# Optimization experiments

Measured on AMD Instinct MI355X. Metric: run time of the kernel, lower is better.

The kernel has to match this reference:

```python
import jax, jax.numpy as jnp
import numpy as np

C = 256
HEADS = 8
HD = C // HEADS
EPS = 1e-5


def _layernorm(x, g, b):
    mu = jnp.mean(x, axis=-1, keepdims=True)
    var = jnp.var(x, axis=-1, keepdims=True)
    return (x - mu) * jax.lax.rsqrt(var + EPS) * g + b


def setup_inputs() -> dict:
    key = jax.random.key(0)
    ks = jax.random.split(key, 16)
    s = 0.02
    return {
        "x": jax.random.normal(ks[0], (1, C, 64, 64), jnp.float32),
        "bn_gamma": 1.0 + s * jax.random.normal(ks[1], (C,), jnp.float32),
        "bn_beta": s * jax.random.normal(ks[2], (C,), jnp.float32),
        "bn_mean": s * jax.random.normal(ks[3], (C,), jnp.float32),
        "bn_var": jnp.ones((C,), jnp.float32),
        "w_in": s * jax.random.normal(ks[4], (C, C), jnp.float32),
        "b_in": jnp.zeros((C,), jnp.float32),
        "ln1_g": jnp.ones((C,), jnp.float32),
        "ln1_b": jnp.zeros((C,), jnp.float32),
        "w_qkv": s * jax.random.normal(ks[5], (3 * C, C), jnp.float32),
        "b_qkv": jnp.zeros((3 * C,), jnp.float32),
        "w_ap": s * jax.random.normal(ks[6], (C, C), jnp.float32),
        "b_ap": jnp.zeros((C,), jnp.float32),
        "ln2_g": jnp.ones((C,), jnp.float32),
        "ln2_b": jnp.zeros((C,), jnp.float32),
        "w_ff1": s * jax.random.normal(ks[7], (4 * C, C), jnp.float32),
        "b_ff1": jnp.zeros((4 * C,), jnp.float32),
        "w_ff2": s * jax.random.normal(ks[8], (C, 4 * C), jnp.float32),
        "b_ff2": jnp.zeros((C,), jnp.float32),
        "w_out": s * jax.random.normal(ks[9], (C, C), jnp.float32),
        "b_out": jnp.zeros((C,), jnp.float32),
    }


def reference(x, bn_gamma, bn_beta, bn_mean, bn_var, w_in, b_in,
              ln1_g, ln1_b, w_qkv, b_qkv, w_ap, b_ap,
              ln2_g, ln2_b, w_ff1, b_ff1, w_ff2, b_ff2, w_out, b_out):
    b, c, h, w = x.shape
    t = h * w
    x_in = x
    # BatchNorm2d (eval mode: running stats)
    xn = (x - bn_mean[None, :, None, None]) * jax.lax.rsqrt(bn_var + EPS)[None, :, None, None]
    xn = xn * bn_gamma[None, :, None, None] + bn_beta[None, :, None, None]
    # proj_in 1x1 conv -> tokens [b, t, c]
    tok = xn.reshape(b, c, t).transpose(0, 2, 1)
    tok = tok @ w_in.T + b_in
    # transformer block (depth=1)
    y = _layernorm(tok, ln1_g, ln1_b)  # norm1
    qkv = y @ w_qkv.T + b_qkv  # [b, t, 3c], channel split (3, H, hd)
    qkv = qkv.reshape(b, t, 3, HEADS, HD)
    q = qkv[:, :, 0].transpose(0, 2, 1, 3)  # [b, H, t, hd]
    k = qkv[:, :, 1].transpose(0, 2, 1, 3)
    v = qkv[:, :, 2].transpose(0, 2, 1, 3)
    scale = HD ** (-0.5)
    attn = jax.nn.softmax(jnp.einsum('bhqd,bhkd->bhqk', q, k) * scale, axis=-1)
    o = jnp.einsum('bhqk,bhkd->bhqd', attn, v)  # [b, H, t, hd]
    o = o.transpose(0, 2, 1, 3).reshape(b, t, c)  # channels ordered (H, hd)
    o = o @ w_ap.T + b_ap  # attn proj 1x1
    attn_out = o + y  # VanillaAttention residual adds its (normed) input
    tok = tok + attn_out
    # FFN
    z = _layernorm(tok, ln2_g, ln2_b)
    z = jax.nn.gelu(z @ w_ff1.T + b_ff1, approximate=False)
    tok = tok + (z @ w_ff2.T + b_ff2)
    # back to image, proj_out 1x1, outer residual
    x4 = tok.transpose(0, 2, 1).reshape(b, c, h, w)
    out = jnp.einsum('oc,bchw->bohw', w_out, x4) + b_out[None, :, None, None]
    return out + x_in
```

## Files before the change

kernel.cpp:

```cpp
#include <hip/hip_runtime.h>
#include <math.h>

#define T_TOK 4096
#define C_DIM 256
#define EPSF  1e-5f
#define SC_QL (0.17677669529663687f * 1.4426950408889634f)

typedef short  bf16x8  __attribute__((ext_vector_type(8)));
typedef float  f32x4   __attribute__((ext_vector_type(4)));
typedef ushort ushort8 __attribute__((ext_vector_type(8)));

__device__ __forceinline__ short f2bf(float f) {
    unsigned u = __builtin_bit_cast(unsigned, f);
    unsigned r = (u + 0x7FFFu + ((u >> 16) & 1u)) >> 16;
    return (short)r;
}
__device__ __forceinline__ unsigned pk_bf16(float a, float b) {
    const unsigned ua = __builtin_bit_cast(unsigned, a) + 0x8000u;
    const unsigned ub = __builtin_bit_cast(unsigned, b) + 0x8000u;
    return __builtin_amdgcn_perm(ub, ua, 0x07060302u);
}

__global__ __launch_bounds__(256) void prep_kernel(
    const float* __restrict__ w_in, const float* __restrict__ w_qkv,
    const float* __restrict__ w_ap, const float* __restrict__ w_ff1,
    const float* __restrict__ w_ff2, const float* __restrict__ w_out,
    const float* __restrict__ b_qkv, ushort* __restrict__ wbuf,
    float* __restrict__ bqs,
    const float* __restrict__ x, const float* __restrict__ gamma,
    const float* __restrict__ beta, const float* __restrict__ mean,
    const float* __restrict__ var, ushort* __restrict__ tin)
{
    __shared__ float tile[32][33];
    if (blockIdx.x < 896) {
        const int gid = blockIdx.x * 256 + threadIdx.x;
        const int e0 = gid * 4;
        const float* src; int off; float sc = 1.f;
        if (e0 < 65536)       { src = w_in;  off = e0; }
        else if (e0 < 262144) { src = w_qkv; off = e0 - 65536; if (off < 65536) sc = SC_QL; }
        else if (e0 < 327680) { src = w_ap;  off = e0 - 262144; }
        else if (e0 < 589824) { src = w_ff1; off = e0 - 327680; }
        else if (e0 < 851968) { src = w_ff2; off = e0 - 589824; }
        else                  { src = w_out; off = e0 - 851968; }
        const float4 v = *(const float4*)(src + off);
        ushort4 o;
        o.x = (ushort)f2bf(v.x * sc); o.y = (ushort)f2bf(v.y * sc);
        o.z = (ushort)f2bf(v.z * sc); o.w = (ushort)f2bf(v.w * sc);
        *(ushort4*)(wbuf + e0) = o;
        if (gid < 192) {
            const float s2 = (gid < 64) ? SC_QL : 1.f;
            float4 b = ((const float4*)b_qkv)[gid];
            b.x *= s2; b.y *= s2; b.z *= s2; b.w *= s2;
            ((float4*)bqs)[gid] = b;
        }
    } else {
        const int bidx = blockIdx.x - 896;
        const int t0 = (bidx & 127) * 32, c0 = (bidx >> 7) * 32;
        const int tx = threadIdx.x & 31, ty = threadIdx.x >> 5;
#pragma unroll
        for (int i = 0; i < 32; i += 8) {
            const int c = c0 + ty + i;
            const float a = rsqrtf(var[c] + EPSF) * gamma[c];
            const float d = beta[c] - mean[c] * a;
            tile[ty + i][tx] = x[c * T_TOK + t0 + tx] * a + d;
        }
        __syncthreads();
#pragma unroll
        for (int i = 0; i < 32; i += 8) {
            const int t = t0 + ty + i;
            tin[t * C_DIM + c0 + tx] = (ushort)f2bf(tile[tx][ty + i]);
        }
    }
}

template <bool WRITE_F32>
__global__ __launch_bounds__(256) void ln_kernel(
    const float* __restrict__ in, const float* __restrict__ g,
    const float* __restrict__ b, float* __restrict__ outF,
    ushort* __restrict__ outB)
{
    const int wave = threadIdx.x >> 6, lane = threadIdx.x & 63;
    const int row = (blockIdx.x << 2) + wave;
    const float4 v = *(const float4*)(in + row * C_DIM + lane * 4);
    float s  = v.x + v.y + v.z + v.w;
    float s2 = v.x * v.x + v.y * v.y + v.z * v.z + v.w * v.w;
#pragma unroll
    for (int off = 32; off > 0; off >>= 1) {
        s  += __shfl_xor(s, off);
        s2 += __shfl_xor(s2, off);
    }
    const float mu  = s * (1.0f / C_DIM);
    const float varr = s2 * (1.0f / C_DIM) - mu * mu;
    const float rs  = rsqrtf(varr + EPSF);
    const float4 gv = *(const float4*)(g + lane * 4);
    const float4 bv = *(const float4*)(b + lane * 4);
    float4 o;
    o.x = (v.x - mu) * rs * gv.x + bv.x;
    o.y = (v.y - mu) * rs * gv.y + bv.y;
    o.z = (v.z - mu) * rs * gv.z + bv.z;
    o.w = (v.w - mu) * rs * gv.w + bv.w;
    if (WRITE_F32) *(float4*)(outF + row * C_DIM + lane * 4) = o;
    ushort4 ob;
    ob.x = (ushort)f2bf(o.x); ob.y = (ushort)f2bf(o.y);
    ob.z = (ushort)f2bf(o.z); ob.w = (ushort)f2bf(o.w);
    *(ushort4*)(outB + row * C_DIM + lane * 4) = ob;
}

template <int MODE>
__global__ __launch_bounds__(512) void gemm_bf(
    const ushort* __restrict__ A, const ushort* __restrict__ W,
    const float* __restrict__ bias, const float* __restrict__ add1,
    const float* __restrict__ add2, const float* __restrict__ xin,
    float* __restrict__ outF, ushort* __restrict__ outB,
    int M, int N, int K)
{
    __shared__ ushort As[2][2][64 * 40];
    __shared__ ushort Ws[2][2][64 * 40];
    __shared__ f32x4  Cred[4][64][4];
    const int m0 = blockIdx.x * 64, n0 = blockIdx.y * 64;
    const int tid = threadIdx.x;
    const int wv = tid >> 6, lane = tid & 63;
    const int half = wv >> 2, wl = wv & 3;
    const int c16 = lane & 15, g = lane >> 4;
    const int ht = tid & 255;
    const int r = ht >> 2, cc8 = (ht & 3) * 8;
    const int Kh = K >> 1;

    const ushort* Ap = A + (size_t)(m0 + r) * K + half * Kh + cc8;
    const ushort* Wp = W + (size_t)(n0 + r) * K + half * Kh + cc8;
    ushort8 apre = *(const ushort8*)Ap;
    ushort8 wpre = *(const ushort8*)Wp;

    f32x4 acc[4] = {};
    int p = 0;
    for (int k0 = 0; k0 < Kh; k0 += 32) {
        *(ushort8*)&As[half][p][r * 40 + cc8] = apre;
        *(ushort8*)&Ws[half][p][r * 40 + cc8] = wpre;
        __syncthreads();
        if (k0 + 32 < Kh) {
            apre = *(const ushort8*)(Ap + k0 + 32);
            wpre = *(const ushort8*)(Wp + k0 + 32);
        }
        const bf16x8 af = *(const bf16x8*)&As[half][p][(wl * 16 + c16) * 40 + g * 8];
#pragma unroll
        for (int nf = 0; nf < 4; ++nf) {
            const bf16x8 bfv = *(const bf16x8*)&Ws[half][p][(nf * 16 + c16) * 40 + g * 8];
            acc[nf] = __builtin_amdgcn_mfma_f32_16x16x32_bf16(af, bfv, acc[nf], 0, 0, 0);
        }
        p ^= 1;
    }

    __syncthreads();
    if (half == 1) {
#pragma unroll
        for (int nf = 0; nf < 4; ++nf) Cred[wl][lane][nf] = acc[nf];
    }
    __syncthreads();
    if (half == 0) {
#pragma unroll
        for (int nf = 0; nf < 4; ++nf) {
            const f32x4 t = Cred[wl][lane][nf];
#pragma unroll
            for (int rr = 0; rr < 4; ++rr) acc[nf][rr] += t[rr];
        }
        const int row0 = m0 + wl * 16 + g * 4;
#pragma unroll
        for (int nf = 0; nf < 4; ++nf) {
            const int col = n0 + nf * 16 + c16;
            const float bc = (MODE == 5) ? 0.f : bias[col];
#pragma unroll
            for (int rr = 0; rr < 4; ++rr) {
                const int row = row0 + rr;
                const size_t idx = (size_t)row * N + col;
                float v = acc[nf][rr] + bc;
                if (MODE == 5) v += bias[row] + xin[idx];
                if (MODE == 2) v += add1[idx] + add2[idx];
                if (MODE == 4) v += add1[idx];
                if (MODE == 3) v = 0.5f * v * (1.0f + erff(v * 0.70710678118654752f));
                if (MODE == 0 || MODE == 2 || MODE == 5) outF[idx] = v;
                else outB[idx] = (ushort)f2bf(v);
            }
        }
    }
}

#define KS   40
#define VTS  72
#define PS_W 36

__global__ __launch_bounds__(256) void attn_mfma(
    const ushort* __restrict__ qkv, ushort* __restrict__ o)
{
    const int h   = blockIdx.y;
    const int q0  = blockIdx.x << 6;
    const int tid = threadIdx.x;
    const int wv  = tid >> 6, lane = tid & 63;
    const int c   = lane & 15, g = lane >> 4;

    __shared__ ushort Ks[2][64 * KS];
    __shared__ ushort Vt[2][32 * VTS];
    __shared__ float  Ps[4][16 * PS_W];

    const bf16x8 qf = *(const bf16x8*)(qkv + (size_t)(q0 + wv * 16 + c) * 768 + h * 32 + g * 8);

    bf16x8 ones;
#pragma unroll
    for (int i = 0; i < 8; ++i) ones[i] = (short)0x3F80;

    f32x4 oacc0 = {0.f, 0.f, 0.f, 0.f};
    f32x4 oacc1 = {0.f, 0.f, 0.f, 0.f};
    f32x4 oaccl = {0.f, 0.f, 0.f, 0.f};

    const int kr = tid >> 2, kc = (tid & 3) * 8;
    const int vp = tid & 31, vd = (tid >> 5) * 4;
    const ushort* kbase = qkv + 256 + h * 32;
    const ushort* vbase = qkv + 512 + h * 32;

    ushort8 kpre  = *(const ushort8*)(kbase + (size_t)kr * 768 + kc);
    ushort4 vpre0 = *(const ushort4*)(vbase + (size_t)(2 * vp) * 768 + vd);
    ushort4 vpre1 = *(const ushort4*)(vbase + (size_t)(2 * vp + 1) * 768 + vd);

    int p = 0;
    for (int kt = 0; kt < 64; ++kt) {
        *(ushort8*)&Ks[p][kr * KS + kc] = kpre;
        {
            unsigned* vtp = (unsigned*)&Vt[p][0];
            vtp[(vd + 0) * (VTS / 2) + vp] = (unsigned)vpre0.x | ((unsigned)vpre1.x << 16);
            vtp[(vd + 1) * (VTS / 2) + vp] = (unsigned)vpre0.y | ((unsigned)vpre1.y << 16);
            vtp[(vd + 2) * (VTS / 2) + vp] = (unsigned)vpre0.z | ((unsigned)vpre1.z << 16);
            vtp[(vd + 3) * (VTS / 2) + vp] = (unsigned)vpre0.w | ((unsigned)vpre1.w << 16);
        }
        __syncthreads();
        if (kt < 63) {
            const size_t t0 = (size_t)(kt + 1) * 64;
            kpre  = *(const ushort8*)(kbase + (t0 + kr) * 768 + kc);
            vpre0 = *(const ushort4*)(vbase + (t0 + 2 * vp) * 768 + vd);
            vpre1 = *(const ushort4*)(vbase + (t0 + 2 * vp + 1) * 768 + vd);
        }

        const ushort* ks = &Ks[p][0];
        const ushort* vt = &Vt[p][0];
        const f32x4 zz = {0.f, 0.f, 0.f, 0.f};
        const bf16x8 k0 = *(const bf16x8*)&ks[(0 * 16 + c) * KS + g * 8];
        const bf16x8 k1 = *(const bf16x8*)&ks[(1 * 16 + c) * KS + g * 8];
        const bf16x8 k2 = *(const bf16x8*)&ks[(2 * 16 + c) * KS + g * 8];
        const bf16x8 k3 = *(const bf16x8*)&ks[(3 * 16 + c) * KS + g * 8];
        const f32x4 s0 = __builtin_amdgcn_mfma_f32_16x16x32_bf16(k0, qf, zz, 0, 0, 0);
        const f32x4 s1 = __builtin_amdgcn_mfma_f32_16x16x32_bf16(k1, qf, zz, 0, 0, 0);
        const f32x4 s2 = __builtin_amdgcn_mfma_f32_16x16x32_bf16(k2, qf, zz, 0, 0, 0);
        const f32x4 s3 = __builtin_amdgcn_mfma_f32_16x16x32_bf16(k3, qf, zz, 0, 0, 0);

        float* prow = &Ps[wv][c * PS_W];
        {
            const float e00 = __builtin_amdgcn_exp2f(s0[0]), e01 = __builtin_amdgcn_exp2f(s0[1]);
            const float e02 = __builtin_amdgcn_exp2f(s0[2]), e03 = __builtin_amdgcn_exp2f(s0[3]);
            const float e10 = __builtin_amdgcn_exp2f(s1[0]), e11 = __builtin_amdgcn_exp2f(s1[1]);
            const float e12 = __builtin_amdgcn_exp2f(s1[2]), e13 = __builtin_amdgcn_exp2f(s1[3]);
            const float e20 = __builtin_amdgcn_exp2f(s2[0]), e21 = __builtin_amdgcn_exp2f(s2[1]);
            const float e22 = __builtin_amdgcn_exp2f(s2[2]), e23 = __builtin_amdgcn_exp2f(s2[3]);
            const float e30 = __builtin_amdgcn_exp2f(s3[0]), e31 = __builtin_amdgcn_exp2f(s3[1]);
            const float e32 = __builtin_amdgcn_exp2f(s3[2]), e33 = __builtin_amdgcn_exp2f(s3[3]);
            prow[0 * 8 + 2 * g + 0] = __builtin_bit_cast(float, pk_bf16(e00, e01));
            prow[0 * 8 + 2 * g + 1] = __builtin_bit_cast(float, pk_bf16(e02, e03));
            prow[1 * 8 + 2 * g + 0] = __builtin_bit_cast(float, pk_bf16(e10, e11));
            prow[1 * 8 + 2 * g + 1] = __builtin_bit_cast(float, pk_bf16(e12, e13));
            prow[2 * 8 + 2 * g + 0] = __builtin_bit_cast(float, pk_bf16(e20, e21));
            prow[2 * 8 + 2 * g + 1] = __builtin_bit_cast(float, pk_bf16(e22, e23));
            prow[3 * 8 + 2 * g + 0] = __builtin_bit_cast(float, pk_bf16(e30, e31));
            prow[3 * 8 + 2 * g + 1] = __builtin_bit_cast(float, pk_bf16(e32, e33));
        }

#pragma unroll
        for (int ch = 0; ch < 2; ++ch) {
            const bf16x8 pf = *(const bf16x8*)&prow[ch * 16 + 4 * g];
            const bf16x8 v0 = *(const bf16x8*)&vt[(c)      * VTS + ch * 32 + g * 8];
            const bf16x8 v1 = *(const bf16x8*)&vt[(16 + c) * VTS + ch * 32 + g * 8];
            oacc0 = __builtin_amdgcn_mfma_f32_16x16x32_bf16(pf, v0, oacc0, 0, 0, 0);
            oacc1 = __builtin_amdgcn_mfma_f32_16x16x32_bf16(pf, v1, oacc1, 0, 0, 0);
            oaccl = __builtin_amdgcn_mfma_f32_16x16x32_bf16(pf, ones, oaccl, 0, 0, 0);
        }
        p ^= 1;
        __syncthreads();
    }

    {
        ushort* op = o + (size_t)(q0 + wv * 16) * 256 + h * 32;
#pragma unroll
        for (int rr = 0; rr < 4; ++rr) {
            const float inv = 1.f / oaccl[rr];
            op[(4 * g + rr) * 256 + c]      = (ushort)f2bf(oacc0[rr] * inv);
            op[(4 * g + rr) * 256 + 16 + c] = (ushort)f2bf(oacc1[rr] * inv);
        }
    }
}

extern "C" void kernel_launch(void* const* d_in, const int* in_sizes, int n_in,
                              void* d_out, int out_size, void* d_ws, size_t ws_size,
                              hipStream_t stream)
{
    const float* x     = (const float*)d_in[0];
    const float* bn_g  = (const float*)d_in[1];
    const float* bn_b  = (const float*)d_in[2];
    const float* bn_m  = (const float*)d_in[3];
    const float* bn_v  = (const float*)d_in[4];
    const float* w_in  = (const float*)d_in[5];
    const float* b_in  = (const float*)d_in[6];
    const float* ln1_g = (const float*)d_in[7];
    const float* ln1_b = (const float*)d_in[8];
    const float* w_qkv = (const float*)d_in[9];
    const float* b_qkv = (const float*)d_in[10];
    const float* w_ap  = (const float*)d_in[11];
    const float* b_ap  = (const float*)d_in[12];
    const float* ln2_g = (const float*)d_in[13];
    const float* ln2_b = (const float*)d_in[14];
    const float* w_ff1 = (const float*)d_in[15];
    const float* b_ff1 = (const float*)d_in[16];
    const float* w_ff2 = (const float*)d_in[17];
    const float* b_ff2 = (const float*)d_in[18];
    const float* w_out = (const float*)d_in[19];
    const float* b_out = (const float*)d_in[20];
    float* out = (float*)d_out;
    float* ws  = (float*)d_ws;

    const size_t MF = 1u << 20;
    float*  tok0    = ws;
    float*  y       = ws + MF;
    float*  tok1    = ws + 2 * MF;
    ushort* qkv_bf  = (ushort*)(ws + 3 * MF);
    ushort* zbuf_bf = (ushort*)(ws + 3 * MF);
    ushort* tin_bf  = (ushort*)(ws + 4 * MF + MF / 2);
    ushort* obuf_bf = tin_bf;
    ushort* y_bf    = (ushort*)(ws + 5 * MF);
    ushort* zin_bf  = y_bf;
    ushort* tok2_bf = (ushort*)(ws + MF);
    ushort* wbuf    = (ushort*)(ws + 5 * MF + MF / 2);
    const ushort* wb_in  = wbuf;
    const ushort* wb_qkv = wbuf + 65536;
    const ushort* wb_ap  = wbuf + 262144;
    const ushort* wb_ff1 = wbuf + 327680;
    const ushort* wb_ff2 = wbuf + 589824;
    const ushort* wb_out = wbuf + 851968;
    float* bqs = (float*)(wbuf + 917504);

    prep_kernel<<<1920, 256, 0, stream>>>(w_in, w_qkv, w_ap, w_ff1, w_ff2, w_out,
                                          b_qkv, wbuf, bqs,
                                          x, bn_g, bn_b, bn_m, bn_v, tin_bf);
    gemm_bf<0><<<dim3(64, 4), 512, 0, stream>>>(tin_bf, wb_in, b_in, nullptr, nullptr, nullptr,
                                                tok0, nullptr, 4096, 256, 256);
    ln_kernel<true><<<1024, 256, 0, stream>>>(tok0, ln1_g, ln1_b, y, y_bf);
    gemm_bf<1><<<dim3(64, 12), 512, 0, stream>>>(y_bf, wb_qkv, bqs, nullptr, nullptr, nullptr,
                                                 nullptr, qkv_bf, 4096, 768, 256);
    attn_mfma<<<dim3(64, 8), 256, 0, stream>>>(qkv_bf, obuf_bf);
    gemm_bf<2><<<dim3(64, 4), 512, 0, stream>>>(obuf_bf, wb_ap, b_ap, y, tok0, nullptr,
                                                tok1, nullptr, 4096, 256, 256);
    ln_kernel<false><<<1024, 256, 0, stream>>>(tok1, ln2_g, ln2_b, nullptr, zin_bf);
    gemm_bf<3><<<dim3(64, 16), 512, 0, stream>>>(zin_bf, wb_ff1, b_ff1, nullptr, nullptr, nullptr,
                                                 nullptr, zbuf_bf, 4096, 1024, 256);
    gemm_bf<4><<<dim3(64, 4), 512, 0, stream>>>(zbuf_bf, wb_ff2, b_ff2, tok1, nullptr, nullptr,
                                                nullptr, tok2_bf, 4096, 256, 1024);
    gemm_bf<5><<<dim3(4, 64), 512, 0, stream>>>(wb_out, tok2_bf, b_out, nullptr, nullptr, x,
                                                out, nullptr, 256, 4096, 256);
}
```

Baseline: 217.4 us.

## Fuse GEMM+LayerNorm chains into three row-tile kernels and split attention over keys

Replaces the separate GEMM and LayerNorm launches with three fused kernels that each process 16-token row tiles: proj_in+LN1+QKV, attn-proj+residual+LN2+FFN1+GELU, and FFN2+residual+proj_out. LayerNorm statistics are reduced in registers with DPP row sums and a small shared buffer. Attention is split across two key halves via a z grid dimension, writing unnormalized partial outputs and row sums that the next kernel combines. This cuts launch count and intermediate round trips and improves attention parallelism. In exchange, weights are read directly from global memory per block without LDS reuse, and only 256 blocks run the fused GEMMs.

Result: no change. 213.9 us (-1.6%).

```diff
diff --git a/kernel.cpp b/kernel.cpp
--- a/kernel.cpp
+++ b/kernel.cpp
@@ -15,11 +15,27 @@
     unsigned r = (u + 0x7FFFu + ((u >> 16) & 1u)) >> 16;
     return (short)r;
 }
+__device__ __forceinline__ float bf2f(ushort u) {
+    return __builtin_bit_cast(float, ((unsigned)u) << 16);
+}
 __device__ __forceinline__ unsigned pk_bf16(float a, float b) {
     const unsigned ua = __builtin_bit_cast(unsigned, a) + 0x8000u;
     const unsigned ub = __builtin_bit_cast(unsigned, b) + 0x8000u;
     return __builtin_amdgcn_perm(ub, ua, 0x07060302u);
 }
+template <int CTRL>
+__device__ __forceinline__ float dppf(float x) {
+    return __builtin_bit_cast(float,
+        __builtin_amdgcn_mov_dpp(__builtin_bit_cast(int, x), CTRL, 0xF, 0xF, true));
+}
+__device__ __forceinline__ float rowsum16(float x) {
+    x += dppf<0xB1>(x);
+    x += dppf<0x4E>(x);
+    x += dppf<0x141>(x);
+    x += dppf<0x140>(x);
+    return x;
+}
+#define MFMA16(a, b, c) __builtin_amdgcn_mfma_f32_16x16x32_bf16(a, b, c, 0, 0, 0)
 
 __global__ __launch_bounds__(256) void prep_kernel(
     const float* __restrict__ w_in, const float* __restrict__ w_qkv,
@@ -73,114 +89,106 @@
     }
 }
 
-template <bool WRITE_F32>
-__global__ __launch_bounds__(256) void ln_kernel(
-    const float* __restrict__ in, const float* __restrict__ g,
-    const float* __restrict__ b, float* __restrict__ outF,
-    ushort* __restrict__ outB)
+__global__ __launch_bounds__(256) void fused_pre(
+    const ushort* __restrict__ tin, const ushort* __restrict__ wb_in,
+    const float* __restrict__ b_in, const float* __restrict__ ln1_g,
+    const float* __restrict__ ln1_b, const ushort* __restrict__ wb_qkv,
+    const float* __restrict__ bqs, float* __restrict__ tok0,
+    float* __restrict__ yout, ushort* __restrict__ qkvb)
 {
-    const int wave = threadIdx.x >> 6, lane = threadIdx.x & 63;
-    const int row = (blockIdx.x << 2) + wave;
-    const float4 v = *(const float4*)(in + row * C_DIM + lane * 4);
-    float s  = v.x + v.y + v.z + v.w;
-    float s2 = v.x * v.x + v.y * v.y + v.z * v.z + v.w * v.w;
-#pragma unroll
-    for (int off = 32; off > 0; off >>= 1) {
-        s  += __shfl_xor(s, off);
-        s2 += __shfl_xor(s2, off);
-    }
-    const float mu  = s * (1.0f / C_DIM);
-    const float varr = s2 * (1.0f / C_DIM) - mu * mu;
-    const float rs  = rsqrtf(varr + EPSF);
-    const float4 gv = *(const float4*)(g + lane * 4);
-    const float4 bv = *(const float4*)(b + lane * 4);
-    float4 o;
-    o.x = (v.x - mu) * rs * gv.x + bv.x;
-    o.y = (v.y - mu) * rs * gv.y + bv.y;
-    o.z = (v.z - mu) * rs * gv.z + bv.z;
-    o.w = (v.w - mu) * rs * gv.w + bv.w;
-    if (WRITE_F32) *(float4*)(outF + row * C_DIM + lane * 4) = o;
-    ushort4 ob;
-    ob.x = (ushort)f2bf(o.x); ob.y = (ushort)f2bf(o.y);
-    ob.z = (ushort)f2bf(o.z); ob.w = (ushort)f2bf(o.w);
-    *(ushort4*)(outB + row * C_DIM + lane * 4) = ob;
-}
-
-template <int MODE>
-__global__ __launch_bounds__(512) void gemm_bf(
-    const ushort* __restrict__ A, const ushort* __restrict__ W,
-    const float* __restrict__ bias, const float* __restrict__ add1,
-    const float* __restrict__ add2, const float* __restrict__ xin,
-    float* __restrict__ outF, ushort* __restrict__ outB,
-    int M, int N, int K)
-{
-    __shared__ ushort As[2][2][64 * 40];
-    __shared__ ushort Ws[2][2][64 * 40];
-    __shared__ f32x4  Cred[4][64][4];
-    const int m0 = blockIdx.x * 64, n0 = blockIdx.y * 64;
-    const int tid = threadIdx.x;
-    const int wv = tid >> 6, lane = tid & 63;
-    const int half = wv >> 2, wl = wv & 3;
-    const int c16 = lane & 15, g = lane >> 4;
-    const int ht = tid & 255;
-    const int r = ht >> 2, cc8 = (ht & 3) * 8;
-    const int Kh = K >> 1;
-
-    const ushort* Ap = A + (size_t)(m0 + r) * K + half * Kh + cc8;
-    const ushort* Wp = W + (size_t)(n0 + r) * K + half * Kh + cc8;
-    ushort8 apre = *(const ushort8*)Ap;
-    ushort8 wpre = *(const ushort8*)Wp;
-
-    f32x4 acc[4] = {};
-    int p = 0;
-    for (int k0 = 0; k0 < Kh; k0 += 32) {
-        *(ushort8*)&As[half][p][r * 40 + cc8] = apre;
-        *(ushort8*)&Ws[half][p][r * 40 + cc8] = wpre;
-        __syncthreads();
-        if (k0 + 32 < Kh) {
-            apre = *(const ushort8*)(Ap + k0 + 32);
-            wpre = *(const ushort8*)(Wp + k0 + 32);
-        }
-        const bf16x8 af = *(const bf16x8*)&As[half][p][(wl * 16 + c16) * 40 + g * 8];
+    __shared__ ushort Atile[16 * 264];
+    __shared__ ushort Ytile[16 * 264];
+    __shared__ float  red[4][16][2];
+    const int t0 = blockIdx.x * 16;
+    const int tid = threadIdx.x, wv = tid >> 6, lane = tid & 63;
+    const int c = lane & 15, g = lane >> 4;
+
+    {
+        const int r = tid >> 4, c0 = (tid & 15) * 16;
+        const ushort8 a0 = *(const ushort8*)(tin + (size_t)(t0 + r) * 256 + c0);
+        const ushort8 a1 = *(const ushort8*)(tin + (size_t)(t0 + r) * 256 + c0 + 8);
+        *(ushort8*)&Atile[r * 264 + c0] = a0;
+        *(ushort8*)&Atile[r * 264 + c0 + 8] = a1;
+    }
+    __syncthreads();
+
+    f32x4 accp[4] = {};
+#pragma unroll 1
+    for (int kc = 0; kc < 8; ++kc) {
+        const bf16x8 af = *(const bf16x8*)&Atile[c * 264 + kc * 32 + g * 8];
 #pragma unroll
         for (int nf = 0; nf < 4; ++nf) {
-            const bf16x8 bfv = *(const bf16x8*)&Ws[half][p][(nf * 16 + c16) * 40 + g * 8];
-            acc[nf] = __builtin_amdgcn_mfma_f32_16x16x32_bf16(af, bfv, acc[nf], 0, 0, 0);
-        }
-        p ^= 1;
-    }
-
-    __syncthreads();
-    if (half == 1) {
-#pragma unroll
-        for (int nf = 0; nf < 4; ++nf) Cred[wl][lane][nf] = acc[nf];
-    }
-    __syncthreads();
-    if (half == 0) {
-#pragma unroll
-        for (int nf = 0; nf < 4; ++nf) {
-            const f32x4 t = Cred[wl][lane][nf];
-#pragma unroll
-            for (int rr = 0; rr < 4; ++rr) acc[nf][rr] += t[rr];
-        }
-        const int row0 = m0 + wl * 16 + g * 4;
-#pragma unroll
-        for (int nf = 0; nf < 4; ++nf) {
-            const int col = n0 + nf * 16 + c16;
-            const float bc = (MODE == 5) ? 0.f : bias[col];
-#pragma unroll
-            for (int rr = 0; rr < 4; ++rr) {
-                const int row = row0 + rr;
-                const size_t idx = (size_t)row * N + col;
-                float v = acc[nf][rr] + bc;
-                if (MODE == 5) v += bias[row] + xin[idx];
-                if (MODE == 2) v += add1[idx] + add2[idx];
-                if (MODE == 4) v += add1[idx];
-                if (MODE == 3) v = 0.5f * v * (1.0f + erff(v * 0.70710678118654752f));
-                if (MODE == 0 || MODE == 2 || MODE == 5) outF[idx] = v;
-                else outB[idx] = (ushort)f2bf(v);
-            }
-        }
+            const bf16x8 bfv = *(const bf16x8*)(wb_in +
+                (size_t)(wv * 64 + nf * 16 + c) * 256 + kc * 32 + g * 8);
+            accp[nf] = MFMA16(af, bfv, accp[nf]);
+        }
+    }
+    float vs[4][4];
+    float s1[4] = {}, s2[4] = {};
+#pragma unroll
+    for (int nf = 0; nf < 4; ++nf) {
+        const int col = wv * 64 + nf * 16 + c;
+        const float bb = b_in[col];
+#pragma unroll
+        for (int rr = 0; rr < 4; ++rr) {
+            const float v = accp[nf][rr] + bb;
+            vs[nf][rr] = v;
+            s1[rr] += v;
+            s2[rr] += v * v;
+            tok0[(size_t)(t0 + 4 * g + rr) * 256 + col] = v;
+        }
+    }
+#pragma unroll
+    for (int rr = 0; rr < 4; ++rr) { s1[rr] = rowsum16(s1[rr]); s2[rr] = rowsum16(s2[rr]); }
+    if (c == 0) {
+#pragma unroll
+        for (int rr = 0; rr < 4; ++rr) {
+            red[wv][4 * g + rr][0] = s1[rr];
+            red[wv][4 * g + rr][1] = s2[rr];
+        }
+    }
+    __syncthreads();
+    float mu[4], rs[4];
+#pragma unroll
+    for (int rr = 0; rr < 4; ++rr) {
+        const int row = 4 * g + rr;
+        const float S  = red[0][row][0] + red[1][row][0] + red[2][row][0] + red[3][row][0];
+        const float S2 = red[0][row][1] + red[1][row][1] + red[2][row][1] + red[3][row][1];
+        mu[rr] = S * (1.0f / 256.0f);
+        const float var = S2 * (1.0f / 256.0f) - mu[rr] * mu[rr];
+        rs[rr] = rsqrtf(var + EPSF);
+    }
+#pragma unroll
+    for (int nf = 0; nf < 4; ++nf) {
+        const int col = wv * 64 + nf * 16 + c;
+        const float gg = ln1_g[col], bb = ln1_b[col];
+#pragma unroll
+        for (int rr = 0; rr < 4; ++rr) {
+            const float yv = (vs[nf][rr] - mu[rr]) * rs[rr] * gg + bb;
+            yout[(size_t)(t0 + 4 * g + rr) * 256 + col] = yv;
+            Ytile[(4 * g + rr) * 264 + col] = (ushort)f2bf(yv);
+        }
+    }
+    __syncthreads();
+
+    f32x4 accq[12] = {};
+#pragma unroll 1
+    for (int kc = 0; kc < 8; ++kc) {
+        const bf16x8 af = *(const bf16x8*)&Ytile[c * 264 + kc * 32 + g * 8];
+#pragma unroll
+        for (int nf = 0; nf < 12; ++nf) {
+            const bf16x8 bfv = *(const bf16x8*)(wb_qkv +
+                (size_t)(wv * 192 + nf * 16 + c) * 256 + kc * 32 + g * 8);
+            accq[nf] = MFMA16(af, bfv, accq[nf]);
+        }
+    }
+#pragma unroll
+    for (int nf = 0; nf < 12; ++nf) {
+        const int col = wv * 192 + nf * 16 + c;
+        const float bb = bqs[col];
+#pragma unroll
+        for (int rr = 0; rr < 4; ++rr)
+            qkvb[(size_t)(t0 + 4 * g + rr) * 768 + col] = (ushort)f2bf(accq[nf][rr] + bb);
     }
 }
 
@@ -189,13 +197,15 @@
 #define PS_W 36
 
 __global__ __launch_bounds__(256) void attn_mfma(
-    const ushort* __restrict__ qkv, ushort* __restrict__ o)
+    const ushort* __restrict__ qkv, ushort* __restrict__ o1,
+    ushort* __restrict__ o2, float* __restrict__ lpart)
 {
-    const int h   = blockIdx.y;
-    const int q0  = blockIdx.x << 6;
-    const int tid = threadIdx.x;
-    const int wv  = tid >> 6, lane = tid & 63;
-    const int c   = lane & 15, g = lane >> 4;
+    const int h    = blockIdx.y;
+    const int q0   = blockIdx.x << 6;
+    const int half = blockIdx.z;
+    const int tid  = threadIdx.x;
+    const int wv   = tid >> 6, lane = tid & 63;
+    const int c    = lane & 15, g = lane >> 4;
 
     __shared__ ushort Ks[2][64 * KS];
     __shared__ ushort Vt[2][32 * VTS];
@@ -216,12 +226,13 @@
     const ushort* kbase = qkv + 256 + h * 32;
     const ushort* vbase = qkv + 512 + h * 32;
 
-    ushort8 kpre  = *(const ushort8*)(kbase + (size_t)kr * 768 + kc);
-    ushort4 vpre0 = *(const ushort4*)(vbase + (size_t)(2 * vp) * 768 + vd);
-    ushort4 vpre1 = *(const ushort4*)(vbase + (size_t)(2 * vp + 1) * 768 + vd);
+    const int kt0 = half * 32, kt1 = kt0 + 32;
+    ushort8 kpre  = *(const ushort8*)(kbase + ((size_t)kt0 * 64 + kr) * 768 + kc);
+    ushort4 vpre0 = *(const ushort4*)(vbase + ((size_t)kt0 * 64 + 2 * vp) * 768 + vd);
+    ushort4 vpre1 = *(const ushort4*)(vbase + ((size_t)kt0 * 64 + 2 * vp + 1) * 768 + vd);
 
     int p = 0;
-    for (int kt = 0; kt < 64; ++kt) {
+    for (int kt = kt0; kt < kt1; ++kt) {
         *(ushort8*)&Ks[p][kr * KS + kc] = kpre;
         {
             unsigned* vtp = (unsigned*)&Vt[p][0];
@@ -231,7 +242,7 @@
             vtp[(vd + 3) * (VTS / 2) + vp] = (unsigned)vpre0.w | ((unsigned)vpre1.w << 16);
         }
         __syncthreads();
-        if (kt < 63) {
+        if (kt + 1 < kt1) {
             const size_t t0 = (size_t)(kt + 1) * 64;
             kpre  = *(const ushort8*)(kbase + (t0 + kr) * 768 + kc);
             vpre0 = *(const ushort4*)(vbase + (t0 + 2 * vp) * 768 + vd);
@@ -245,10 +256,10 @@
         const bf16x8 k1 = *(const bf16x8*)&ks[(1 * 16 + c) * KS + g * 8];
         const bf16x8 k2 = *(const bf16x8*)&ks[(2 * 16 + c) * KS + g * 8];
         const bf16x8 k3 = *(const bf16x8*)&ks[(3 * 16 + c) * KS + g * 8];
-        const f32x4 s0 = __builtin_amdgcn_mfma_f32_16x16x32_bf16(k0, qf, zz, 0, 0, 0);
-        const f32x4 s1 = __builtin_amdgcn_mfma_f32_16x16x32_bf16(k1, qf, zz, 0, 0, 0);
-        const f32x4 s2 = __builtin_amdgcn_mfma_f32_16x16x32_bf16(k2, qf, zz, 0, 0, 0);
-        const f32x4 s3 = __builtin_amdgcn_mfma_f32_16x16x32_bf16(k3, qf, zz, 0, 0, 0);
+        const f32x4 s0 = MFMA16(k0, qf, zz);
+        const f32x4 s1 = MFMA16(k1, qf, zz);
+        const f32x4 s2 = MFMA16(k2, qf, zz);
+        const f32x4 s3 = MFMA16(k3, qf, zz);
 
         float* prow = &Ps[wv][c * PS_W];
         {
@@ -269,27 +280,224 @@
             prow[3 * 8 + 2 * g + 0] = __builtin_bit_cast(float, pk_bf16(e30, e31));
             prow[3 * 8 + 2 * g + 1] = __builtin_bit_cast(float, pk_bf16(e32, e33));
         }
-
 #pragma unroll
         for (int ch = 0; ch < 2; ++ch) {
             const bf16x8 pf = *(const bf16x8*)&prow[ch * 16 + 4 * g];
             const bf16x8 v0 = *(const bf16x8*)&vt[(c)      * VTS + ch * 32 + g * 8];
             const bf16x8 v1 = *(const bf16x8*)&vt[(16 + c) * VTS + ch * 32 + g * 8];
-            oacc0 = __builtin_amdgcn_mfma_f32_16x16x32_bf16(pf, v0, oacc0, 0, 0, 0);
-            oacc1 = __builtin_amdgcn_mfma_f32_16x16x32_bf16(pf, v1, oacc1, 0, 0, 0);
-            oaccl = __builtin_amdgcn_mfma_f32_16x16x32_bf16(pf, ones, oaccl, 0, 0, 0);
+            oacc0 = MFMA16(pf, v0, oacc0);
+            oacc1 = MFMA16(pf, v1, oacc1);
+            oaccl = MFMA16(pf, ones, oaccl);
         }
         p ^= 1;
         __syncthreads();
     }
 
     {
-        ushort* op = o + (size_t)(q0 + wv * 16) * 256 + h * 32;
-#pragma unroll
-        for (int rr = 0; rr < 4; ++rr) {
-            const float inv = 1.f / oaccl[rr];
-            op[(4 * g + rr) * 256 + c]      = (ushort)f2bf(oacc0[rr] * inv);
-            op[(4 * g + rr) * 256 + 16 + c] = (ushort)f2bf(oacc1[rr] * inv);
+        ushort* op = (half ? o2 : o1) + (size_t)(q0 + wv * 16) * 256 + h * 32;
+#pragma unroll
+        for (int rr = 0; rr < 4; ++rr) {
+            op[(4 * g + rr) * 256 + c]      = (ushort)f2bf(oacc0[rr]);
+            op[(4 * g + rr) * 256 + 16 + c] = (ushort)f2bf(oacc1[rr]);
+        }
+        if (c == 0) {
+#pragma unroll
+            for (int rr = 0; rr < 4; ++rr)
+                lpart[(size_t)(q0 + wv * 16 + 4 * g + rr) * 16 + half * 8 + h] = oaccl[rr];
+        }
+    }
+}
+
+__global__ __launch_bounds__(256) void fused_mid(
+    const ushort* __restrict__ o1, const ushort* __restrict__ o2,
+    const float* __restrict__ lpart, const ushort* __restrict__ wb_ap,
+    const float* __restrict__ b_ap, const float* __restrict__ yin,
+    const float* __restrict__ tok0, const float* __restrict__ ln2_g,
+    const float* __restrict__ ln2_b, const ushort* __restrict__ wb_ff1,
+    const float* __restrict__ b_ff1, float* __restrict__ tok1,
+    ushort* __restrict__ zbuf)
+{
+    __shared__ ushort Otile[16 * 264];
+    __shared__ ushort Ztile[16 * 264];
+    __shared__ float  red[4][16][2];
+    const int t0 = blockIdx.x * 16;
+    const int tid = threadIdx.x, wv = tid >> 6, lane = tid & 63;
+    const int c = lane & 15, g = lane >> 4;
+
+    {
+        const int r = tid >> 4, c0 = (tid & 15) * 16;
+        const int h = (tid & 15) >> 1;
+        const float inv = 1.0f / (lpart[(size_t)(t0 + r) * 16 + h] +
+                                  lpart[(size_t)(t0 + r) * 16 + 8 + h]);
+        const ushort8 a0 = *(const ushort8*)(o1 + (size_t)(t0 + r) * 256 + c0);
+        const ushort8 a1 = *(const ushort8*)(o1 + (size_t)(t0 + r) * 256 + c0 + 8);
+        const ushort8 b0 = *(const ushort8*)(o2 + (size_t)(t0 + r) * 256 + c0);
+        const ushort8 b1 = *(const ushort8*)(o2 + (size_t)(t0 + r) * 256 + c0 + 8);
+        unsigned w[4];
+#pragma unroll
+        for (int i = 0; i < 4; ++i) {
+            const float v0 = (bf2f(a0[2 * i]) + bf2f(b0[2 * i])) * inv;
+            const float v1 = (bf2f(a0[2 * i + 1]) + bf2f(b0[2 * i + 1])) * inv;
+            w[i] = pk_bf16(v0, v1);
+        }
+        *(ushort8*)&Otile[r * 264 + c0] = *(ushort8*)w;
+#pragma unroll
+        for (int i = 0; i < 4; ++i) {
+            const float v0 = (bf2f(a1[2 * i]) + bf2f(b1[2 * i])) * inv;
+            const float v1 = (bf2f(a1[2 * i + 1]) + bf2f(b1[2 * i + 1])) * inv;
+            w[i] = pk_bf16(v0, v1);
+        }
+        *(ushort8*)&Otile[r * 264 + c0 + 8] = *(ushort8*)w;
+    }
+    __syncthreads();
+
+    f32x4 accp[4] = {};
+#pragma unroll 1
+    for (int kc = 0; kc < 8; ++kc) {
+        const bf16x8 af = *(const bf16x8*)&Otile[c * 264 + kc * 32 + g * 8];
+#pragma unroll
+        for (int nf = 0; nf < 4; ++nf) {
+            const bf16x8 bfv = *(const bf16x8*)(wb_ap +
+                (size_t)(wv * 64 + nf * 16 + c) * 256 + kc * 32 + g * 8);
+            accp[nf] = MFMA16(af, bfv, accp[nf]);
+        }
+    }
+    float vs[4][4];
+    float s1[4] = {}, s2[4] = {};
+#pragma unroll
+    for (int nf = 0; nf < 4; ++nf) {
+        const int col = wv * 64 + nf * 16 + c;
+        const float bb = b_ap[col];
+#pragma unroll
+        for (int rr = 0; rr < 4; ++rr) {
+            const size_t idx = (size_t)(t0 + 4 * g + rr) * 256 + col;
+            const float v = accp[nf][rr] + bb + yin[idx] + tok0[idx];
+            vs[nf][rr] = v;
+            s1[rr] += v;
+            s2[rr] += v * v;
+            tok1[idx] = v;
+        }
+    }
+#pragma unroll
+    for (int rr = 0; rr < 4; ++rr) { s1[rr] = rowsum16(s1[rr]); s2[rr] = rowsum16(s2[rr]); }
+    if (c == 0) {
+#pragma unroll
+        for (int rr = 0; rr < 4; ++rr) {
+            red[wv][4 * g + rr][0] = s1[rr];
+            red[wv][4 * g + rr][1] = s2[rr];
+        }
+    }
+    __syncthreads();
+    float mu[4], rs[4];
+#pragma unroll
+    for (int rr = 0; rr < 4; ++rr) {
+        const int row = 4 * g + rr;
+        const float S  = red[0][row][0] + red[1][row][0] + red[2][row][0] + red[3][row][0];
+        const float S2 = red[0][row][1] + red[1][row][1] + red[2][row][1] + red[3][row][1];
+        mu[rr] = S * (1.0f / 256.0f);
+        const float var = S2 * (1.0f / 256.0f) - mu[rr] * mu[rr];
+        rs[rr] = rsqrtf(var + EPSF);
+    }
+#pragma unroll
+    for (int nf = 0; nf < 4; ++nf) {
+        const int col = wv * 64 + nf * 16 + c;
+        const float gg = ln2_g[col], bb = ln2_b[col];
+#pragma unroll
+        for (int rr = 0; rr < 4; ++rr) {
+            const float zv = (vs[nf][rr] - mu[rr]) * rs[rr] * gg + bb;
+            Ztile[(4 * g + rr) * 264 + col] = (ushort)f2bf(zv);
+        }
+    }
+    __syncthreads();
+
+    f32x4 accf[16] = {};
+#pragma unroll 1
+    for (int kc = 0; kc < 8; ++kc) {
+        const bf16x8 af = *(const bf16x8*)&Ztile[c * 264 + kc * 32 + g * 8];
+#pragma unroll
+        for (int nf = 0; nf < 16; ++nf) {
+            const bf16x8 bfv = *(const bf16x8*)(wb_ff1 +
+                (size_t)(wv * 256 + nf * 16 + c) * 256 + kc * 32 + g * 8);
+            accf[nf] = MFMA16(af, bfv, accf[nf]);
+        }
+    }
+#pragma unroll
+    for (int nf = 0; nf < 16; ++nf) {
+        const int col = wv * 256 + nf * 16 + c;
+        const float bb = b_ff1[col];
+#pragma unroll
+        for (int rr = 0; rr < 4; ++rr) {
+            float v = accf[nf][rr] + bb;
+            v = 0.5f * v * (1.0f + erff(v * 0.70710678118654752f));
+            zbuf[(size_t)(t0 + 4 * g + rr) * 1024 + col] = (ushort)f2bf(v);
+        }
+    }
+}
+
+__global__ __launch_bounds__(256) void fused_post(
+    const ushort* __restrict__ zbuf, const ushort* __restrict__ wb_ff2,
+    const float* __restrict__ b_ff2, const float* __restrict__ tok1,
+    const ushort* __restrict__ wb_out, const float* __restrict__ b_out,
+    const float* __restrict__ x, float* __restrict__ out)
+{
+    __shared__ ushort Ztile[16 * 1032];
+    __shared__ ushort T2tile[16 * 264];
+    const int t0 = blockIdx.x * 16;
+    const int tid = threadIdx.x, wv = tid >> 6, lane = tid & 63;
+    const int c = lane & 15, g = lane >> 4;
+
+    {
+        const int r = tid >> 4, c0 = (tid & 15) * 64;
+#pragma unroll
+        for (int i = 0; i < 8; ++i) {
+            const ushort8 zv = *(const ushort8*)(zbuf + (size_t)(t0 + r) * 1024 + c0 + i * 8);
+            *(ushort8*)&Ztile[r * 1032 + c0 + i * 8] = zv;
+        }
+    }
+    __syncthreads();
+
+    f32x4 accf[4] = {};
+#pragma unroll 1
+    for (int kc = 0; kc < 32; ++kc) {
+        const bf16x8 af = *(const bf16x8*)&Ztile[c * 1032 + kc * 32 + g * 8];
+#pragma unroll
+        for (int nf = 0; nf < 4; ++nf) {
+            const bf16x8 bfv = *(const bf16x8*)(wb_ff2 +
+                (size_t)(wv * 64 + nf * 16 + c) * 1024 + kc * 32 + g * 8);
+            accf[nf] = MFMA16(af, bfv, accf[nf]);
+        }
+    }
+#pragma unroll
+    for (int nf = 0; nf < 4; ++nf) {
+        const int col = wv * 64 + nf * 16 + c;
+        const float bb = b_ff2[col];
+#pragma unroll
+        for (int rr = 0; rr < 4; ++rr) {
+            const size_t idx = (size_t)(t0 + 4 * g + rr) * 256 + col;
+            const float v = accf[nf][rr] + bb + tok1[idx];
+            T2tile[(4 * g + rr) * 264 + col] = (ushort)f2bf(v);
+        }
+    }
+    __syncthreads();
+
+    f32x4 acco[4] = {};
+#pragma unroll 1
+    for (int kc = 0; kc < 8; ++kc) {
+        const bf16x8 bfr = *(const bf16x8*)&T2tile[c * 264 + kc * 32 + g * 8];
+#pragma unroll
+        for (int mf = 0; mf < 4; ++mf) {
+            const bf16x8 afr = *(const bf16x8*)(wb_out +
+                (size_t)(wv * 64 + mf * 16 + c) * 256 + kc * 32 + g * 8);
+            acco[mf] = MFMA16(afr, bfr, acco[mf]);
+        }
+    }
+#pragma unroll
+    for (int mf = 0; mf < 4; ++mf) {
+#pragma unroll
+        for (int rr = 0; rr < 4; ++rr) {
+            const int och = wv * 64 + mf * 16 + 4 * g + rr;
+            const size_t idx = (size_t)och * T_TOK + t0 + c;
+            out[idx] = acco[mf][rr] + b_out[och] + x[idx];
         }
     }
 }
@@ -323,17 +531,16 @@
     float* ws  = (float*)d_ws;
 
     const size_t MF = 1u << 20;
-    float*  tok0    = ws;
-    float*  y       = ws + MF;
-    float*  tok1    = ws + 2 * MF;
-    ushort* qkv_bf  = (ushort*)(ws + 3 * MF);
-    ushort* zbuf_bf = (ushort*)(ws + 3 * MF);
-    ushort* tin_bf  = (ushort*)(ws + 4 * MF + MF / 2);
-    ushort* obuf_bf = tin_bf;
-    ushort* y_bf    = (ushort*)(ws + 5 * MF);
-    ushort* zin_bf  = y_bf;
-    ushort* tok2_bf = (ushort*)(ws + MF);
-    ushort* wbuf    = (ushort*)(ws + 5 * MF + MF / 2);
+    float*  tok0   = ws;
+    float*  y      = ws + MF;
+    float*  tok1   = ws + 2 * MF;
+    ushort* qkv_bf = (ushort*)(ws + 3 * MF);
+    ushort* zbuf   = (ushort*)(ws + 4 * MF + MF / 2);
+    ushort* tin_bf = (ushort*)(ws + 6 * MF + MF / 2);
+    ushort* o1p    = tin_bf;
+    ushort* o2p    = (ushort*)(ws + 7 * MF);
+    float*  lpart  = ws + 7 * MF + MF / 2;
+    ushort* wbuf   = (ushort*)(ws + 7 * MF + MF / 2 + 65536);
     const ushort* wb_in  = wbuf;
     const ushort* wb_qkv = wbuf + 65536;
     const ushort* wb_ap  = wbuf + 262144;
@@ -345,19 +552,11 @@
     prep_kernel<<<1920, 256, 0, stream>>>(w_in, w_qkv, w_ap, w_ff1, w_ff2, w_out,
                                           b_qkv, wbuf, bqs,
                                           x, bn_g, bn_b, bn_m, bn_v, tin_bf);
-    gemm_bf<0><<<dim3(64, 4), 512, 0, stream>>>(tin_bf, wb_in, b_in, nullptr, nullptr, nullptr,
-                                                tok0, nullptr, 4096, 256, 256);
-    ln_kernel<true><<<1024, 256, 0, stream>>>(tok0, ln1_g, ln1_b, y, y_bf);
-    gemm_bf<1><<<dim3(64, 12), 512, 0, stream>>>(y_bf, wb_qkv, bqs, nullptr, nullptr, nullptr,
-                                                 nullptr, qkv_bf, 4096, 768, 256);
-    attn_mfma<<<dim3(64, 8), 256, 0, stream>>>(qkv_bf, obuf_bf);
-    gemm_bf<2><<<dim3(64, 4), 512, 0, stream>>>(obuf_bf, wb_ap, b_ap, y, tok0, nullptr,
-                                                tok1, nullptr, 4096, 256, 256);
-    ln_kernel<false><<<1024, 256, 0, stream>>>(tok1, ln2_g, ln2_b, nullptr, zin_bf);
-    gemm_bf<3><<<dim3(64, 16), 512, 0, stream>>>(zin_bf, wb_ff1, b_ff1, nullptr, nullptr, nullptr,
-                                                 nullptr, zbuf_bf, 4096, 1024, 256);
-    gemm_bf<4><<<dim3(64, 4), 512, 0, stream>>>(zbuf_bf, wb_ff2, b_ff2, tok1, nullptr, nullptr,
-                                                nullptr, tok2_bf, 4096, 256, 1024);
-    gemm_bf<5><<<dim3(4, 64), 512, 0, stream>>>(wb_out, tok2_bf, b_out, nullptr, nullptr, x,
-                                                out, nullptr, 256, 4096, 256);
-}
+    fused_pre<<<256, 256, 0, stream>>>(tin_bf, wb_in, b_in, ln1_g, ln1_b,
+                                       wb_qkv, bqs, tok0, y, qkv_bf);
+    attn_mfma<<<dim3(64, 8, 2), 256, 0, stream>>>(qkv_bf, o1p, o2p, lpart);
+    fused_mid<<<256, 256, 0, stream>>>(o1p, o2p, lpart, wb_ap, b_ap, y, tok0,
+                                       ln2_g, ln2_b, wb_ff1, b_ff1, tok1, zbuf);
+    fused_post<<<256, 256, 0, stream>>>(zbuf, wb_ff2, b_ff2, tok1, wb_out, b_out,
+                                        x, out);
+}
```
